# Kernel tuning notes

Hardware: AMD Instinct MI355X
Metric: run time of the kernel (lower is better)

The kernel has to match this reference:

```python
import jax, jax.numpy as jnp
import numpy as np

EPS = 1e-5

def _layernorm(x, w, b):
    mu = jnp.mean(x, axis=-1, keepdims=True)
    var = jnp.mean((x - mu) ** 2, axis=-1, keepdims=True)
    return (x - mu) * jax.lax.rsqrt(var + EPS) * w + b

def _ssm(x, in_proj_w, x_proj_w, dt_proj_w, dt_proj_b, conv1d_w, conv1d_b,
         A_log, D, out_proj_w, norm_w, norm_b, d_state=16):
    # x: (B, L, d_model)
    xz = jnp.einsum('bld,ed->ble', x, in_proj_w)          # (B,L,2*d_inner)
    d_inner = xz.shape[-1] // 2
    x_in, z = xz[..., :d_inner], xz[..., d_inner:]
    # depthwise conv1d, kernel 3, pad 1
    xc = jax.lax.conv_general_dilated(
        jnp.transpose(x_in, (0, 2, 1)), conv1d_w,
        window_strides=(1,), padding=((1, 1),),
        feature_group_count=d_inner,
        dimension_numbers=('NCH', 'OIH', 'NCH'))
    xc = jnp.transpose(xc, (0, 2, 1)) + conv1d_b          # (B,L,d_inner)
    xc = jax.nn.silu(xc)
    dbc = jnp.einsum('bld,ed->ble', xc, x_proj_w)         # (B,L,1+2*d_state)
    delta = dbc[..., :1]
    B_mat = dbc[..., 1:1 + d_state]
    C_mat = dbc[..., 1 + d_state:]
    delta = jax.nn.softplus(jnp.einsum('blo,eo->ble', delta, dt_proj_w) + dt_proj_b)  # (B,L,d_inner)
    A = -jnp.exp(A_log)                                   # (d_inner,d_state)
    dA = jnp.exp(delta[..., None] * A[None, None])        # (B,L,d_inner,d_state)
    xbu = delta[..., None] * B_mat[:, :, None, :] * xc[..., None]
    def combine(c1, c2):
        a1, b1 = c1
        a2, b2 = c2
        return (a2 * a1, b2 + a2 * b1)
    _, h = jax.lax.associative_scan(combine, (dA, xbu), axis=1)  # h_t = dA_t h_{t-1} + xbu_t, h_0=0
    y = jnp.sum(h * C_mat[:, :, None, :], axis=-1)        # (B,L,d_inner)
    y = y + xc * D
    y = y * jax.nn.silu(z)
    y = _layernorm(y, norm_w, norm_b)
    return jnp.einsum('ble,de->bld', y, out_proj_w)

def reference(x, in_proj_w, x_proj_w, dt_proj_w, dt_proj_b, conv1d_w, conv1d_b,
              A_log, D, out_proj_w, norm_ssm_w, norm_ssm_b, norm1_w, norm1_b,
              dw_w, dw_b, gate):
    B, C, H, W = x.shape
    # local branch: depthwise 7x7 conv
    local = jax.lax.conv_general_dilated(
        x, dw_w, window_strides=(1, 1), padding=((3, 3), (3, 3)),
        feature_group_count=C, dimension_numbers=('NCHW', 'OIHW', 'NCHW'))
    local = local + dw_b[None, :, None, None]
    L = H * W
    max_seq_len = 256
    if L <= max_seq_len:
        x_flat = jnp.transpose(x, (0, 2, 3, 1)).reshape(B, L, C)
        ssm_out = _ssm(_layernorm(x_flat, norm1_w, norm1_b), in_proj_w, x_proj_w,
                       dt_proj_w, dt_proj_b, conv1d_w, conv1d_b, A_log, D,
                       out_proj_w, norm_ssm_w, norm_ssm_b)
        ssm_out = jnp.transpose(ssm_out.reshape(B, H, W, C), (0, 3, 1, 2))
    else:
        scale = (max_seq_len / L) ** 0.5
        h_s = max(1, int(H * scale))
        w_s = max(1, int(W * scale))
        # adaptive avg pool; H,W chosen divisible by h_s,w_s -> exact block mean
        x_small = x.reshape(B, C, h_s, H // h_s, w_s, W // w_s).mean(axis=(3, 5))
        x_flat = jnp.transpose(x_small, (0, 2, 3, 1)).reshape(B, h_s * w_s, C)
        ssm_small = _ssm(_layernorm(x_flat, norm1_w, norm1_b), in_proj_w, x_proj_w,
                         dt_proj_w, dt_proj_b, conv1d_w, conv1d_b, A_log, D,
                         out_proj_w, norm_ssm_w, norm_ssm_b)
        ssm_small = jnp.transpose(ssm_small.reshape(B, h_s, w_s, C), (0, 3, 1, 2))
        ssm_out = jax.image.resize(ssm_small, (B, C, H, W), method='bilinear')  # align_corners=False
    g = jax.nn.sigmoid(gate[0])
    return x + g * ssm_out + (1.0 - g) * local

def setup_inputs() -> dict:
    key = jax.random.key(0)
    ks = jax.random.split(key, 8)
    C, d_state, d_inner = 192, 16, 384
    Bsz, H, W = 32, 64, 64
    s = 0.02
    A = jnp.broadcast_to(jnp.arange(1, d_state + 1, dtype=jnp.float32), (d_inner, d_state))
    return {
        'x': jax.random.normal(ks[0], (Bsz, C, H, W), jnp.float32),
        'in_proj_w': jax.random.normal(ks[1], (2 * d_inner, C), jnp.float32) * s,
        'x_proj_w': jax.random.normal(ks[2], (2 * d_state + 1, d_inner), jnp.float32) * s,
        'dt_proj_w': jax.random.normal(ks[3], (d_inner, 1), jnp.float32) * s,
        'dt_proj_b': jnp.zeros((d_inner,), jnp.float32),
        'conv1d_w': jax.random.normal(ks[4], (d_inner, 1, 3), jnp.float32) * 0.2,
        'conv1d_b': jnp.zeros((d_inner,), jnp.float32),
        'A_log': jnp.log(A),
        'D': jnp.ones((d_inner,), jnp.float32),
        'out_proj_w': jax.random.normal(ks[5], (C, d_inner), jnp.float32) * s,
        'norm_ssm_w': jnp.ones((d_inner,), jnp.float32),
        'norm_ssm_b': jnp.zeros((d_inner,), jnp.float32),
        'norm1_w': jnp.ones((C,), jnp.float32),
        'norm1_b': jnp.zeros((C,), jnp.float32),
        'dw_w': jax.random.normal(ks[6], (C, 1, 7, 7), jnp.float32) * 0.05,
        'dw_b': jnp.zeros((C,), jnp.float32),
        'gate': jnp.ones((1,), jnp.float32),
    }
```

## Files before the change

kernel.cpp:

```cpp
#include <hip/hip_runtime.h>
#include <stdint.h>

#define B_   32
#define C_   192
#define Hh   64
#define Ww   64
#define LS   256
#define DI   384
#define DSt  16
#define E2   768

__global__ __launch_bounds__(256) void k_pool_ln(
    const float* __restrict__ x, const float* __restrict__ w, const float* __restrict__ bb,
    float* __restrict__ xln)
{
  int b = blockIdx.x >> 4, i = blockIdx.x & 15;
  int tid = threadIdx.x;
  int wv = tid >> 6;
  int off = tid & 63;
  int j = off & 15;

  __shared__ float pooledT[16 * 193];
  __shared__ float red1[4][16], red2[4][16];
  __shared__ float muL[16], rsL[16];

  const float* xbase = x + (((size_t)(b * C_) * Hh + i * 4) * Ww);
#pragma unroll 4
  for (int cc = 0; cc < 48; ++cc) {
    int c = cc * 4 + wv;
    float4 v = *reinterpret_cast<const float4*>(xbase + (size_t)c * (Hh * Ww) + off * 4);
    float s = v.x + v.y + v.z + v.w;
    s += __shfl_xor(s, 16, 64);
    s += __shfl_xor(s, 32, 64);
    if (off < 16) pooledT[j * 193 + c] = s * (1.f / 16.f);
  }
  __syncthreads();

  int j2 = tid & 15, cg = tid >> 4;
  float s1 = 0.f, s2 = 0.f;
#pragma unroll
  for (int ccx = 0; ccx < 12; ++ccx) {
    float v = pooledT[j2 * 193 + cg * 12 + ccx];
    s1 += v; s2 += v * v;
  }
  s1 += __shfl_xor(s1, 16, 64); s1 += __shfl_xor(s1, 32, 64);
  s2 += __shfl_xor(s2, 16, 64); s2 += __shfl_xor(s2, 32, 64);
  if ((tid & 63) < 16) { red1[tid >> 6][j2] = s1; red2[tid >> 6][j2] = s2; }
  __syncthreads();
  if (tid < 16) {
    float t1 = red1[0][tid] + red1[1][tid] + red1[2][tid] + red1[3][tid];
    float t2 = red2[0][tid] + red2[1][tid] + red2[2][tid] + red2[3][tid];
    float mu = t1 / 192.f;
    float var = t2 / 192.f - mu * mu;
    muL[tid] = mu; rsL[tid] = rsqrtf(var + 1e-5f);
  }
  __syncthreads();

#pragma unroll
  for (int k = 0; k < 12; ++k) {
    int o = tid + 256 * k;
    int c = o % 192, jj = o / 192;
    float v = (pooledT[jj * 193 + c] - muL[jj]) * rsL[jj] * w[c] + bb[c];
    xln[((size_t)(b * 256 + i * 16 + jj)) * C_ + c] = v;
  }
}

__global__ __launch_bounds__(256) void k_gemm_f32(
    const float* __restrict__ A, const float* __restrict__ W,
    float* __restrict__ C, int N, int K)
{
  __shared__ float At[8][132];
  __shared__ float Wt[8][132];
  int tid = threadIdx.x;
  int m0 = blockIdx.y * 128, n0 = blockIdx.x * 128;
  int tx = tid & 15, ty = tid >> 4;
  int lr = tid >> 1, lk = (tid & 1) * 4;
  float acc[8][8] = {};
  const float* Arow = A + (size_t)(m0 + lr) * K + lk;
  int wrow = n0 + lr; if (wrow >= N) wrow = N - 1;
  const float* Wrow = W + (size_t)wrow * K + lk;
  for (int k0 = 0; k0 < K; k0 += 8) {
    float4 av = *reinterpret_cast<const float4*>(Arow + k0);
    float4 wv = *reinterpret_cast<const float4*>(Wrow + k0);
    __syncthreads();
    At[lk + 0][lr] = av.x; At[lk + 1][lr] = av.y; At[lk + 2][lr] = av.z; At[lk + 3][lr] = av.w;
    Wt[lk + 0][lr] = wv.x; Wt[lk + 1][lr] = wv.y; Wt[lk + 2][lr] = wv.z; Wt[lk + 3][lr] = wv.w;
    __syncthreads();
#pragma unroll
    for (int k = 0; k < 8; ++k) {
      float4 a0 = *reinterpret_cast<const float4*>(&At[k][8 * ty]);
      float4 a1 = *reinterpret_cast<const float4*>(&At[k][8 * ty + 4]);
      float4 w0 = *reinterpret_cast<const float4*>(&Wt[k][8 * tx]);
      float4 w1 = *reinterpret_cast<const float4*>(&Wt[k][8 * tx + 4]);
      float a[8] = {a0.x, a0.y, a0.z, a0.w, a1.x, a1.y, a1.z, a1.w};
      float w[8] = {w0.x, w0.y, w0.z, w0.w, w1.x, w1.y, w1.z, w1.w};
#pragma unroll
      for (int i = 0; i < 8; ++i)
#pragma unroll
        for (int j = 0; j < 8; ++j) acc[i][j] += a[i] * w[j];
    }
  }
#pragma unroll
  for (int i = 0; i < 8; ++i) {
    int row = m0 + 8 * ty + i;
    int col0 = n0 + 8 * tx;
    if (col0 < N)
      *reinterpret_cast<float4*>(C + (size_t)row * N + col0) =
          make_float4(acc[i][0], acc[i][1], acc[i][2], acc[i][3]);
    if (col0 + 4 < N)
      *reinterpret_cast<float4*>(C + (size_t)row * N + col0 + 4) =
          make_float4(acc[i][4], acc[i][5], acc[i][6], acc[i][7]);
  }
}

__global__ __launch_bounds__(256) void k_conv_silu(
    const float* __restrict__ xz, const float* __restrict__ cw, const float* __restrict__ cb,
    float* __restrict__ xc)
{
  int idx = blockIdx.x * 256 + threadIdx.x;
  int e = idx % DI;
  int row = idx / DI;
  int l = row & 255;
  const float* xin = xz + (size_t)row * E2 + e;
  float x0 = *xin;
  float xm = (l > 0)   ? *(xin - E2) : 0.f;
  float xp = (l < 255) ? *(xin + E2) : 0.f;
  float v = cw[e * 3 + 0] * xm + cw[e * 3 + 1] * x0 + cw[e * 3 + 2] * xp + cb[e];
  xc[idx] = v / (1.f + expf(-v));
}

__global__ __launch_bounds__(256) void k_xproj(
    const float* __restrict__ xc, const float* __restrict__ xw,
    const float* __restrict__ dtw, const float* __restrict__ dtb,
    float* __restrict__ BC, float* __restrict__ delta)
{
  int wid = threadIdx.x >> 6, lane = threadIdx.x & 63;
  int row = blockIdx.x * 4 + wid;
  const float* xr = xc + (size_t)row * DI;
  float xv[6];
#pragma unroll
  for (int k = 0; k < 6; ++k) xv[k] = xr[lane + 64 * k];
  float dres = 0.f, mine = 0.f;
  for (int j = 0; j < 33; ++j) {
    const float* wr = xw + (size_t)j * DI;
    float p = 0.f;
#pragma unroll
    for (int k = 0; k < 6; ++k) p += wr[lane + 64 * k] * xv[k];
#pragma unroll
    for (int off = 32; off; off >>= 1) p += __shfl_xor(p, off, 64);
    if (j == 0) dres = p;
    else if (lane == j - 1) mine = p;
  }
  if (lane < 32) BC[(size_t)row * 32 + lane] = mine;
#pragma unroll
  for (int k = 0; k < 6; ++k) {
    int e = lane + 64 * k;
    float dr = dres * dtw[e] + dtb[e];
    delta[(size_t)row * DI + e] = dr > 20.f ? dr : log1pf(expf(dr));
  }
}

__global__ __launch_bounds__(256) void k_scan(
    const float* __restrict__ delta, const float* __restrict__ xc,
    const float* __restrict__ BC, const float* __restrict__ xz,
    const float* __restrict__ A_log, const float* __restrict__ Dp,
    float* __restrict__ yg)
{
  int blk = blockIdx.x;
  int b = blk / 24, eg = blk - b * 24;
  int tid = threadIdx.x;
  int et = tid >> 4, s = tid & 15;
  int e = eg * 16 + et;
  float Aes = -expf(A_log[e * DSt + s]);
  float Dv = Dp[e];
  size_t rbase = (size_t)b * 256;
  const float* pd = delta + rbase * DI + e;
  const float* px = xc + rbase * DI + e;
  const float* pb = BC + rbase * 32 + s;
  const float* pz = xz + rbase * E2 + DI + e;
  float* py = yg + rbase * DI + e;

  float dv = pd[0], xcv = px[0], Bm = pb[0], Cm = pb[16], zv = pz[0];
  float h = 0.f;
#pragma unroll 4
  for (int l = 0; l < 256; ++l) {
    float dv_n = 0.f, xcv_n = 0.f, Bm_n = 0.f, Cm_n = 0.f, zv_n = 0.f;
    if (l < 255) {
      size_t r = (size_t)(l + 1);
      dv_n  = pd[r * DI];
      xcv_n = px[r * DI];
      Bm_n  = pb[r * 32];
      Cm_n  = pb[r * 32 + 16];
      zv_n  = pz[r * E2];
    }
    float da = expf(dv * Aes);
    h = da * h + dv * Bm * xcv;
    float contrib = h * Cm;
    contrib += __shfl_xor(contrib, 1, 64);
    contrib += __shfl_xor(contrib, 2, 64);
    contrib += __shfl_xor(contrib, 4, 64);
    contrib += __shfl_xor(contrib, 8, 64);
    if (s == 0) {
      float y = (contrib + xcv * Dv) * (zv / (1.f + expf(-zv)));
      py[(size_t)l * DI] = y;
    }
    dv = dv_n; xcv = xcv_n; Bm = Bm_n; Cm = Cm_n; zv = zv_n;
  }
}

__global__ __launch_bounds__(128) void k_ln_ssm(
    const float* __restrict__ yg, const float* __restrict__ nw, const float* __restrict__ nb,
    float* __restrict__ yn)
{
  int row = blockIdx.x;
  int t = threadIdx.x;
  const float* yr = yg + (size_t)row * DI;
  float v0 = yr[t], v1 = yr[t + 128], v2 = yr[t + 256];
  float s1 = v0 + v1 + v2, s2 = v0 * v0 + v1 * v1 + v2 * v2;
#pragma unroll
  for (int off = 32; off; off >>= 1) {
    s1 += __shfl_xor(s1, off, 64);
    s2 += __shfl_xor(s2, off, 64);
  }
  __shared__ float a1[2], a2[2];
  if ((t & 63) == 0) { a1[t >> 6] = s1; a2[t >> 6] = s2; }
  __syncthreads();
  float t1 = a1[0] + a1[1], t2 = a2[0] + a2[1];
  float mu = t1 / 384.f, var = t2 / 384.f - mu * mu;
  float rstd = rsqrtf(var + 1e-5f);
  float* yo = yn + (size_t)row * DI;
  yo[t]       = (v0 - mu) * rstd * nw[t]       + nb[t];
  yo[t + 128] = (v1 - mu) * rstd * nw[t + 128] + nb[t + 128];
  yo[t + 256] = (v2 - mu) * rstd * nw[t + 256] + nb[t + 256];
}

__global__ __launch_bounds__(256) void k_final(
    const float* __restrict__ x, const float* __restrict__ dww, const float* __restrict__ dwb,
    const float* __restrict__ ssm, const float* __restrict__ gate,
    float* __restrict__ out)
{
  int blk = blockIdx.x;
  int ti = blk & 3;
  int c = (blk >> 2) % C_;
  int b = blk / (4 * C_);
  int h0 = ti * 16;
  __shared__ float xpatch[22 * 72];
  __shared__ float wlds[49];
  __shared__ float slds[6 * 16];
  __shared__ float biass;
  int tid = threadIdx.x;
  if (tid < 49) wlds[tid] = dww[(size_t)c * 49 + tid];
  if (tid == 49) biass = dwb[c];
  int ibase = (h0 >> 2) - 1;
  if (tid < 96) {
    int ii = ibase + (tid >> 4);
    ii = ii < 0 ? 0 : (ii > 15 ? 15 : ii);
    int jj = tid & 15;
    slds[tid] = ssm[((size_t)(b * LS) + ii * 16 + jj) * C_ + c];
  }
  const float* xb = x + ((size_t)(b * C_ + c) * Hh) * Ww;
  for (int idx = tid; idx < 22 * 70; idx += 256) {
    int r = idx / 70, col = idx % 70;
    int gh = h0 - 3 + r, gw = col - 3;
    float v = 0.f;
    if (gh >= 0 && gh < 64 && gw >= 0 && gw < 64)
      v = xb[gh * 64 + gw];
    xpatch[r * 72 + col] = v;
  }
  __syncthreads();
  float g = 1.f / (1.f + expf(-gate[0]));
  int qn = tid >> 5;
  int R0 = qn * 2;
  int w0 = (tid & 31) * 2;
  float a00 = 0, a01 = 0, a10 = 0, a11 = 0;
#pragma unroll
  for (int k = 0; k < 8; ++k) {
    const float* prow = &xpatch[(R0 + k) * 72 + w0];
    float v[8];
#pragma unroll
    for (int d = 0; d < 8; ++d) v[d] = prow[d];
    if (k < 7) {
#pragma unroll
      for (int dx = 0; dx < 7; ++dx) {
        float wv = wlds[k * 7 + dx];
        a00 += wv * v[dx]; a01 += wv * v[dx + 1];
      }
    }
    if (k > 0) {
#pragma unroll
      for (int dx = 0; dx < 7; ++dx) {
        float wv = wlds[(k - 1) * 7 + dx];
        a10 += wv * v[dx]; a11 += wv * v[dx + 1];
      }
    }
  }
  float locs[2][2] = {{a00 + biass, a01 + biass}, {a10 + biass, a11 + biass}};
  float* orow = out + ((size_t)(b * C_ + c) * Hh) * Ww;
#pragma unroll
  for (int rr = 0; rr < 2; ++rr) {
    int hgl = h0 + R0 + rr;
    float ci = hgl * 0.25f - 0.375f;
    float fif = floorf(ci);
    int i0 = (int)fif;
    float fi = ci - fif;
    int li = i0 - ibase;
    const float* r0p = &slds[li * 16];
    const float* r1p = &slds[(li + 1) * 16];
    float ov[2];
#pragma unroll
    for (int ccx = 0; ccx < 2; ++ccx) {
      int wgl = w0 + ccx;
      float cj = wgl * 0.25f - 0.375f;
      float fjf = floorf(cj);
      int j0 = (int)fjf;
      float fj = cj - fjf;
      int jc0 = j0 < 0 ? 0 : j0;
      int jc1 = (j0 + 1) > 15 ? 15 : (j0 + 1);
      float sv = (1.f - fi) * ((1.f - fj) * r0p[jc0] + fj * r0p[jc1])
               +         fi * ((1.f - fj) * r1p[jc0] + fj * r1p[jc1]);
      float xv = xpatch[(R0 + rr + 3) * 72 + (wgl + 3)];
      ov[ccx] = xv + g * sv + (1.f - g) * locs[rr][ccx];
    }
    *reinterpret_cast<float2*>(&orow[hgl * 64 + w0]) = make_float2(ov[0], ov[1]);
  }
}

extern "C" void kernel_launch(void* const* d_in, const int* in_sizes, int n_in,
                              void* d_out, int out_size, void* d_ws, size_t ws_size,
                              hipStream_t stream)
{
  const float* x    = (const float*)d_in[0];
  const float* inw  = (const float*)d_in[1];
  const float* xw   = (const float*)d_in[2];
  const float* dtw  = (const float*)d_in[3];
  const float* dtb  = (const float*)d_in[4];
  const float* cw   = (const float*)d_in[5];
  const float* cb   = (const float*)d_in[6];
  const float* alog = (const float*)d_in[7];
  const float* Dp   = (const float*)d_in[8];
  const float* ow   = (const float*)d_in[9];
  const float* nsw  = (const float*)d_in[10];
  const float* nsb  = (const float*)d_in[11];
  const float* n1w  = (const float*)d_in[12];
  const float* n1b  = (const float*)d_in[13];
  const float* dww  = (const float*)d_in[14];
  const float* dwb  = (const float*)d_in[15];
  const float* gate = (const float*)d_in[16];

  char* ws = (char*)d_ws;
  float* xln   = (float*)ws; ws += (size_t)8192 * 192 * 4;
  float* xz    = (float*)ws; ws += (size_t)8192 * 768 * 4;
  float* xc    = (float*)ws; ws += (size_t)8192 * 384 * 4;
  float* delta = (float*)ws; ws += (size_t)8192 * 384 * 4;
  float* BC    = (float*)ws; ws += (size_t)8192 * 32 * 4;
  float* yg    = (float*)ws; ws += (size_t)8192 * 384 * 4;
  float* yn  = xz;
  float* ssm = xln;

  k_pool_ln<<<B_ * 16, 256, 0, stream>>>(x, n1w, n1b, xln);
  k_gemm_f32<<<dim3(6, 64), 256, 0, stream>>>(xln, inw, xz, 768, 192);
  k_conv_silu<<<12288, 256, 0, stream>>>(xz, cw, cb, xc);
  k_xproj<<<2048, 256, 0, stream>>>(xc, xw, dtw, dtb, BC, delta);
  k_scan<<<B_ * 24, 256, 0, stream>>>(delta, xc, BC, xz, alog, Dp, yg);
  k_ln_ssm<<<8192, 128, 0, stream>>>(yg, nsw, nsb, yn);
  k_gemm_f32<<<dim3(2, 64), 256, 0, stream>>>(yn, ow, ssm, 192, 384);
  k_final<<<24576, 256, 0, stream>>>(x, dww, dwb, ssm, gate, (float*)d_out);
}
```

Measured before the change: 523.0 us.

## Batch scan loads in chunks of 16 and reduce state via LDS transpose

The selective-scan kernel now loads 16 timesteps of delta, x, B and C into registers at once, runs the sequential recurrence over them, and writes the per-state contributions to shared memory. After a barrier, each thread sums one timestep's 16 state contributions, so every lane performs the gating and store instead of only lane zero. This replaces the four-step shuffle reduction and the single-step prefetch with deeper memory-level parallelism and fully parallel epilogue work. In exchange it adds two block barriers per chunk, uses more registers, and switches to fast __expf intrinsics.

Result: faster. 477.7 us (-8.6%).

```diff
diff --git a/kernel.cpp b/kernel.cpp
--- a/kernel.cpp
+++ b/kernel.cpp
@@ -172,39 +172,48 @@
   int et = tid >> 4, s = tid & 15;
   int e = eg * 16 + et;
   float Aes = -expf(A_log[e * DSt + s]);
-  float Dv = Dp[e];
-  size_t rbase = (size_t)b * 256;
-  const float* pd = delta + rbase * DI + e;
-  const float* px = xc + rbase * DI + e;
-  const float* pb = BC + rbase * 32 + s;
-  const float* pz = xz + rbase * E2 + DI + e;
-  float* py = yg + rbase * DI + e;
-
-  float dv = pd[0], xcv = px[0], Bm = pb[0], Cm = pb[16], zv = pz[0];
+  float Dv16 = Dp[e] * (1.f / 16.f);
+
+  const float* dbase  = delta + (size_t)b * 256 * DI;
+  const float* xbase  = xc    + (size_t)b * 256 * DI;
+  const float* bcbase = BC    + (size_t)b * 256 * 32;
+  const float* zbase  = xz    + (size_t)b * 256 * E2 + DI;
+  float*       ybase  = yg    + (size_t)b * 256 * DI;
+
+  __shared__ float tr[16 * 16 * 20];
+  float* myw = &tr[(et * 16) * 20 + s];
+  const float* myr = &tr[(et * 16 + s) * 20];
+
   float h = 0.f;
-#pragma unroll 4
-  for (int l = 0; l < 256; ++l) {
-    float dv_n = 0.f, xcv_n = 0.f, Bm_n = 0.f, Cm_n = 0.f, zv_n = 0.f;
-    if (l < 255) {
-      size_t r = (size_t)(l + 1);
-      dv_n  = pd[r * DI];
-      xcv_n = px[r * DI];
-      Bm_n  = pb[r * 32];
-      Cm_n  = pb[r * 32 + 16];
-      zv_n  = pz[r * E2];
-    }
-    float da = expf(dv * Aes);
-    h = da * h + dv * Bm * xcv;
-    float contrib = h * Cm;
-    contrib += __shfl_xor(contrib, 1, 64);
-    contrib += __shfl_xor(contrib, 2, 64);
-    contrib += __shfl_xor(contrib, 4, 64);
-    contrib += __shfl_xor(contrib, 8, 64);
-    if (s == 0) {
-      float y = (contrib + xcv * Dv) * (zv / (1.f + expf(-zv)));
-      py[(size_t)l * DI] = y;
-    }
-    dv = dv_n; xcv = xcv_n; Bm = Bm_n; Cm = Cm_n; zv = zv_n;
+  for (int g = 0; g < 16; ++g) {
+    int l0 = g * 16;
+    float dv[16], xv[16], Bm[16], Cm[16];
+#pragma unroll
+    for (int i = 0; i < 16; ++i) {
+      int row = l0 + i;
+      dv[i] = dbase[row * DI + e];
+      xv[i] = xbase[row * DI + e];
+      Bm[i] = bcbase[row * 32 + s];
+      Cm[i] = bcbase[row * 32 + 16 + s];
+    }
+    __syncthreads();
+#pragma unroll
+    for (int i = 0; i < 16; ++i) {
+      float da = __expf(dv[i] * Aes);
+      h = da * h + dv[i] * Bm[i] * xv[i];
+      myw[i * 20] = h * Cm[i] + xv[i] * Dv16;
+    }
+    __syncthreads();
+    float4 p0 = *reinterpret_cast<const float4*>(myr + 0);
+    float4 p1 = *reinterpret_cast<const float4*>(myr + 4);
+    float4 p2 = *reinterpret_cast<const float4*>(myr + 8);
+    float4 p3 = *reinterpret_cast<const float4*>(myr + 12);
+    float S = ((p0.x + p0.y) + (p0.z + p0.w)) + ((p1.x + p1.y) + (p1.z + p1.w))
+            + ((p2.x + p2.y) + (p2.z + p2.w)) + ((p3.x + p3.y) + (p3.z + p3.w));
+    int l = l0 + s;
+    float zv = zbase[l * E2 + e];
+    float y = S * (zv / (1.f + __expf(-zv)));
+    ybase[l * DI + e] = y;
   }
 }
 
```
